# Kernel tuning notes

Measured on AMD Instinct MI355X. Metric: run time of the kernel, lower is better.

The kernel has to match this reference:

```python
import jax, jax.numpy as jnp
import numpy as np

NS = 100000  # senders
NR = 100000  # receivers
E = 600000   # edges
D = 128      # sender_dim = receiver_dim = edge_dim
EPS = 1e-5


def _layer_norm(x, g, b):
    mu = jnp.mean(x, axis=-1, keepdims=True)
    var = jnp.mean(jnp.square(x - mu), axis=-1, keepdims=True)
    return (x - mu) * jax.lax.rsqrt(var + EPS) * g + b


def _gcast_mlp(x, W, b, gamma, beta):
    # Faithful to GCastMLP.forward: z = silu(linear(x)); z = LN(silu(z))
    z = jax.nn.silu(x @ W.T + b)
    return _layer_norm(jax.nn.silu(z), gamma, beta)


def setup_inputs() -> dict:
    key = jax.random.key(0)
    ks = jax.random.split(key, 12)
    s = 1.0 / np.sqrt(3 * D)
    inp = {
        "sender_x": jax.random.normal(ks[0], (NS, D), jnp.float32),
        "receiver_x": jax.random.normal(ks[1], (NR, D), jnp.float32),
        "edge_index": jax.random.randint(ks[2], (2, E), 0, NR, jnp.int32),
        "edge_attr": jax.random.normal(ks[3], (E, D), jnp.float32),
        # edge MLP: in = sender+receiver+edge = 3D, out = edge_dim
        "We": jax.random.uniform(ks[4], (D, 3 * D), jnp.float32, -s, s),
        "be": jnp.zeros((D,), jnp.float32),
        "ge": jnp.ones((D,), jnp.float32),
        "bbe": jnp.zeros((D,), jnp.float32),
        # node MLP: in = receiver+edge = 2D, out = receiver_dim
        "Wn": jax.random.uniform(ks[5], (D, 2 * D), jnp.float32, -1.0 / np.sqrt(2 * D), 1.0 / np.sqrt(2 * D)),
        "bn": jnp.zeros((D,), jnp.float32),
        "gn": jnp.ones((D,), jnp.float32),
        "bbn": jnp.zeros((D,), jnp.float32),
        # sender MLP: square D -> D
        "Ws": jax.random.uniform(ks[6], (D, D), jnp.float32, -1.0 / np.sqrt(D), 1.0 / np.sqrt(D)),
        "bs": jnp.zeros((D,), jnp.float32),
        "gs": jnp.ones((D,), jnp.float32),
        "bbs": jnp.zeros((D,), jnp.float32),
    }
    return inp


def reference(sender_x, receiver_x, edge_index, edge_attr,
              We, be, ge, bbe, Wn, bn, gn, bbn, Ws, bs, gs, bbs):
    src, dst = edge_index[0], edge_index[1]
    # Edge encoder: gather endpoints, concat, MLP -> new edge features [E, D]
    edge_in = jnp.concatenate([sender_x[src], receiver_x[dst], edge_attr], axis=-1)
    edge_attr_p = _gcast_mlp(edge_in, We, be, ge, bbe)
    # Node encoder: scatter-sum messages (= new edge features) to receivers
    edge_aggr = jax.ops.segment_sum(edge_attr_p, dst, num_segments=receiver_x.shape[0])
    mesh_x_p = _gcast_mlp(jnp.concatenate([receiver_x, edge_aggr], axis=-1), Wn, bn, gn, bbn)
    # Residual updates
    sender_out = sender_x + _gcast_mlp(sender_x, Ws, bs, gs, bbs)
    receiver_out = receiver_x + mesh_x_p
    edge_out = edge_attr + edge_attr_p
    return (sender_out, receiver_out, edge_out)
```

## Files before the change

kernel.cpp:

```cpp
#include <hip/hip_runtime.h>
#include <stdint.h>


typedef __bf16 bf16x8 __attribute__((ext_vector_type(8)));
typedef float  f32x4  __attribute__((ext_vector_type(4)));

union U16B { uint4 u; bf16x8 v; };
union BFPK { __bf16 h[2]; unsigned int u; };
union BF1  { __bf16 h; unsigned short s; };

__device__ __forceinline__ float silu_f(float x) {
  return x * __builtin_amdgcn_rcpf(1.0f + __expf(-x));
}
__device__ __forceinline__ float bfu2f(unsigned int lo16) {
  return __uint_as_float(lo16 << 16);
}
__device__ __forceinline__ bf16x8 cvt8(float4 a, float4 b) {
  bf16x8 r;
  r[0] = (__bf16)a.x; r[1] = (__bf16)a.y; r[2] = (__bf16)a.z; r[3] = (__bf16)a.w;
  r[4] = (__bf16)b.x; r[5] = (__bf16)b.y; r[6] = (__bf16)b.z; r[7] = (__bf16)b.w;
  return r;
}

__global__ void prep_kernel(const float* __restrict__ We,
                            const float* __restrict__ Wn,
                            const float* __restrict__ Ws,
                            unsigned short* __restrict__ wimg,
                            const float* __restrict__ sx,
                            unsigned short* __restrict__ sb,
                            const float* __restrict__ rx,
                            unsigned short* __restrict__ rb,
                            int n8s, int n8r,
                            const int* __restrict__ dst,
                            int* __restrict__ counts, int E) {
  int i = blockIdx.x * 256 + threadIdx.x;
  if (i < 6 * 16384) {
    int panel = i >> 14;
    int r = (i >> 7) & 127;
    int csw = i & 127;
    int c_or = ((csw * 2) ^ ((r & 15) << 4)) >> 1;
    float f;
    if (panel < 3)      f = We[r * 384 + panel * 128 + c_or];
    else if (panel < 5) f = Wn[r * 256 + (panel - 3) * 128 + c_or];
    else                f = Ws[r * 128 + c_or];
    BF1 c; c.h = (__bf16)f;
    wimg[i] = c.s;
    return;
  }
  int j = i - 6 * 16384;
  if (j < n8s + n8r) {
    const float* in; unsigned short* out; int idx;
    if (j < n8s) { in = sx; out = sb; idx = j; }
    else         { in = rx; out = rb; idx = j - n8s; }
    float4 a = reinterpret_cast<const float4*>(in)[2 * idx];
    float4 b = reinterpret_cast<const float4*>(in)[2 * idx + 1];
    U16B r8; r8.v = cvt8(a, b);
    reinterpret_cast<uint4*>(out)[idx] = r8.u;
    return;
  }
  int e = j - n8s - n8r;
  if (e < E) atomicAdd(&counts[dst[e]], 1);
}

__global__ void scan1_kernel(const int* __restrict__ counts, int* __restrict__ pre,
                             int* __restrict__ blockSums, int n) {
  __shared__ int sh[256];
  const int t = threadIdx.x;
  const int base = blockIdx.x * 1024 + t * 4;
  int c0 = (base + 0 < n) ? counts[base + 0] : 0;
  int c1 = (base + 1 < n) ? counts[base + 1] : 0;
  int c2 = (base + 2 < n) ? counts[base + 2] : 0;
  int c3 = (base + 3 < n) ? counts[base + 3] : 0;
  int tot = c0 + c1 + c2 + c3;
  sh[t] = tot;
  __syncthreads();
  #pragma unroll
  for (int off = 1; off < 256; off <<= 1) {
    int v = (t >= off) ? sh[t - off] : 0;
    __syncthreads();
    sh[t] += v;
    __syncthreads();
  }
  int excl = sh[t] - tot;
  if (base + 0 < n) pre[base + 0] = excl;
  if (base + 1 < n) pre[base + 1] = excl + c0;
  if (base + 2 < n) pre[base + 2] = excl + c0 + c1;
  if (base + 3 < n) pre[base + 3] = excl + c0 + c1 + c2;
  if (t == 255) blockSums[blockIdx.x] = sh[255];
}

__global__ void scan2_kernel(int* __restrict__ blockSums, int nb) {
  __shared__ int sh[512];
  const int t = threadIdx.x;
  int v = (t < nb) ? blockSums[t] : 0;
  sh[t] = v;
  __syncthreads();
  #pragma unroll
  for (int off = 1; off < 512; off <<= 1) {
    int u = (t >= off) ? sh[t - off] : 0;
    __syncthreads();
    sh[t] += u;
    __syncthreads();
  }
  if (t < nb) blockSums[t] = sh[t] - v;
}

__global__ void scan3_kernel(const int* __restrict__ pre, const int* __restrict__ blockSums,
                             int* __restrict__ offs, int* __restrict__ cursor, int n) {
  int i = blockIdx.x * 256 + threadIdx.x;
  if (i >= n) return;
  int o = pre[i] + blockSums[i >> 10];
  offs[i] = o;
  cursor[i] = o;
}

__global__ void scatter_kernel(const int* __restrict__ dst, int* __restrict__ cursor,
                               int* __restrict__ rank, int E) {
  int i = blockIdx.x * 256 + threadIdx.x;
  if (i < E) {
    int p = atomicAdd(&cursor[dst[i]], 1);
    rank[i] = p;
  }
}

template <int KDIM, int AGGR>
__device__ __forceinline__ void mlp_core(
    unsigned short* smem,
    const unsigned short* __restrict__ s0, const int* __restrict__ i0,
    const unsigned short* __restrict__ s1, const int* __restrict__ i1,
    const float* __restrict__ s2,
    const unsigned short* __restrict__ Wb,
    const float* __restrict__ bias, const float* __restrict__ gamma,
    const float* __restrict__ beta,
    const float* __restrict__ resid,
    float* __restrict__ outp,
    void* aggr, const int* __restrict__ aggr_idx,
    const int* __restrict__ prank,
    int M, int bid) {
  constexpr int NSEG = KDIM / 128;

  const int tid = threadIdx.x;
  const int wid = tid >> 6;
  const int lane = tid & 63;
  const int l15 = lane & 15;
  const int q = lane >> 4;
  const int l31 = lane & 31;
  const int rhalf = lane >> 5;
  const int wrow = bid * 128 + wid * 16;
  const int xm = l15 << 3;

  int rr = wrow + l15;
  if (rr >= M) rr = M - 1;
  const unsigned short* p0 = s0 + (size_t)(i0 ? i0[rr] : rr) * 128;
  const unsigned short* p1 = nullptr;
  const float* p2 = nullptr;
  if constexpr (KDIM >= 256) p1 = s1 + (size_t)(i1 ? i1[rr] : rr) * 128;
  if constexpr (KDIM >= 384) p2 = s2 + (size_t)rr * 128;

  auto stageB = [&](int seg) {
    const unsigned short* g = Wb + seg * 16384 + wid * 2048 + lane * 8;
    unsigned short* l = &smem[wid * 2048];
    #pragma unroll
    for (int u = 0; u < 4; ++u) {
      __builtin_amdgcn_global_load_lds(
          (const __attribute__((address_space(1))) unsigned int*)(g + u * 512),
          (__attribute__((address_space(3))) unsigned int*)(l + u * 512),
          16, 0, 0);
    }
  };

  U16B Ac[4], An[4];
  auto loadA = [&](int seg, U16B (&dst)[4]) {
    #pragma unroll
    for (int k4 = 0; k4 < 4; ++k4) {
      const int kof = k4 * 32 + q * 8;
      if (seg == 0) {
        dst[k4].u = *reinterpret_cast<const uint4*>(p0 + kof);
      } else if (seg == 1) {
        dst[k4].u = *reinterpret_cast<const uint4*>(p1 + kof);
      } else {
        const float4* p = reinterpret_cast<const float4*>(p2 + kof);
        dst[k4].v = cvt8(p[0], p[1]);
      }
    }
  };

  f32x4 acc[8] = {};

  stageB(0);
  loadA(0, Ac);
  __syncthreads();

  #pragma unroll
  for (int seg = 0; seg < NSEG; ++seg) {
    if (seg + 1 < NSEG) loadA(seg + 1, An);
    #pragma unroll
    for (int k4 = 0; k4 < 4; ++k4) {
      #pragma unroll
      for (int n = 0; n < 8; ++n) {
        U16B b;
        b.u = *reinterpret_cast<const uint4*>(
            &smem[(n * 16 + l15) * 128 + ((k4 * 32 + q * 8) ^ xm)]);
        acc[n] = __builtin_amdgcn_mfma_f32_16x16x32_bf16(Ac[k4].v, b.v, acc[n], 0, 0, 0);
      }
    }
    __syncthreads();
    if (seg + 1 < NSEG) {
      stageB(seg + 1);
      __syncthreads();
      #pragma unroll
      for (int k4 = 0; k4 < 4; ++k4) Ac[k4] = An[k4];
    }
  }

  float bia[8];
  #pragma unroll
  for (int n = 0; n < 8; ++n) bia[n] = bias[n * 16 + l15];

  float sum[4] = {0.f, 0.f, 0.f, 0.f};
  float ssq[4] = {0.f, 0.f, 0.f, 0.f};
  #pragma unroll
  for (int n = 0; n < 8; ++n) {
    #pragma unroll
    for (int j = 0; j < 4; ++j) {
      float t = silu_f(silu_f(acc[n][j] + bia[n]));
      acc[n][j] = t;
      sum[j] += t;
      ssq[j] += t * t;
    }
  }
  #pragma unroll
  for (int off = 1; off < 16; off <<= 1) {
    #pragma unroll
    for (int j = 0; j < 4; ++j) {
      sum[j] += __shfl_xor(sum[j], off);
      ssq[j] += __shfl_xor(ssq[j], off);
    }
  }
  float mu[4], rs[4];
  #pragma unroll
  for (int j = 0; j < 4; ++j) {
    mu[j] = sum[j] * (1.0f / 128.0f);
    float var = ssq[j] * (1.0f / 128.0f) - mu[j] * mu[j];
    rs[j] = rsqrtf(var + 1e-5f);
  }
  float gam[8], bet[8];
  #pragma unroll
  for (int n = 0; n < 8; ++n) {
    gam[n] = gamma[n * 16 + l15];
    bet[n] = beta[n * 16 + l15];
  }

  unsigned short* yw = &smem[wid * 2048];

  #pragma unroll
  for (int h = 0; h < 2; ++h) {
    if (h == 1) {
      asm volatile("s_waitcnt lgkmcnt(0)" ::: "memory");
    }
    if ((q >> 1) == h) {
      #pragma unroll
      for (int n = 0; n < 8; ++n) {
        #pragma unroll
        for (int j = 0; j < 4; ++j) {
          float y = (acc[n][j] - mu[j]) * rs[j] * gam[n] + bet[n];
          BF1 c; c.h = (__bf16)y;
          yw[((q & 1) * 4 + j) * 132 + n * 16 + l15] = c.s;
        }
      }
    }
    asm volatile("s_waitcnt lgkmcnt(0)" ::: "memory");

    #pragma unroll
    for (int s = 0; s < 4; ++s) {
      int row8 = 2 * s + rhalf;
      int grow = wrow + 8 * h + row8;
      uint2 w = *reinterpret_cast<const uint2*>(&yw[row8 * 132 + l31 * 4]);
      if (grow < M) {
        const f32x4 r4 = *reinterpret_cast<const f32x4*>(resid + (size_t)grow * 128 + l31 * 4);
        f32x4 o4;
        o4.x = r4.x + bfu2f(w.x & 0xffffu);
        o4.y = r4.y + bfu2f(w.x >> 16);
        o4.z = r4.z + bfu2f(w.y & 0xffffu);
        o4.w = r4.w + bfu2f(w.y >> 16);
        __builtin_nontemporal_store(o4, reinterpret_cast<f32x4*>(outp + (size_t)grow * 128 + l31 * 4));
        if constexpr (AGGR == 3) {
          int prow = prank[grow];
          *reinterpret_cast<uint2*>((unsigned short*)aggr + (size_t)prow * 128 + l31 * 4) = w;
        } else if constexpr (AGGR == 2) {
          int idx = aggr_idx[grow];
          unsigned short* ar = (unsigned short*)aggr + (size_t)idx * 128 + l31 * 4;
          asm volatile("global_atomic_pk_add_bf16 %0, %1, off" :: "v"(ar), "v"(w.x) : "memory");
          asm volatile("global_atomic_pk_add_bf16 %0, %1, off" :: "v"(ar + 2), "v"(w.y) : "memory");
        }
      }
    }
  }
}

template <int KDIM, int AGGR>
__global__ __launch_bounds__(512, 6) void mlp_v10_kernel(
    const unsigned short* __restrict__ s0, const int* __restrict__ i0,
    const unsigned short* __restrict__ s1, const int* __restrict__ i1,
    const float* __restrict__ s2,
    const unsigned short* __restrict__ Wb,
    const float* __restrict__ bias, const float* __restrict__ gamma,
    const float* __restrict__ beta,
    const float* __restrict__ resid,
    float* __restrict__ outp,
    void* aggr, const int* __restrict__ aggr_idx,
    const int* __restrict__ prank,
    int M) {
  __shared__ __align__(16) unsigned short smem[16384];
  mlp_core<KDIM, AGGR>(smem, s0, i0, s1, i1, s2, Wb, bias, gamma, beta,
                       resid, outp, aggr, aggr_idx, prank, M, blockIdx.x);
}

__global__ __launch_bounds__(512, 6) void fused_es_kernel(
    const unsigned short* __restrict__ sender_b, const int* __restrict__ src,
    const unsigned short* __restrict__ receiver_b, const int* __restrict__ dst,
    const float* __restrict__ edge_attr,
    const unsigned short* __restrict__ We_b,
    const float* __restrict__ be, const float* __restrict__ ge,
    const float* __restrict__ bbe,
    float* __restrict__ edge_out,
    unsigned short* __restrict__ P, const int* __restrict__ rank,
    const unsigned short* __restrict__ Ws_b,
    const float* __restrict__ bs, const float* __restrict__ gs,
    const float* __restrict__ bbs,
    const float* __restrict__ sender_x, float* __restrict__ sender_out,
    int E, int NS, int gridE) {
  __shared__ __align__(16) unsigned short smem[16384];
  const int b = blockIdx.x;
  if (b < gridE) {
    mlp_core<384, 3>(smem, sender_b, src, receiver_b, dst, edge_attr,
                     We_b, be, ge, bbe, edge_attr, edge_out,
                     P, nullptr, rank, E, b);
  } else {
    mlp_core<128, 0>(smem, sender_b, nullptr, nullptr, nullptr, nullptr,
                     Ws_b, bs, gs, bbs, sender_x, sender_out,
                     nullptr, nullptr, nullptr, NS, b - gridE);
  }
}

__global__ __launch_bounds__(512, 4) void node_csr_kernel(
    const unsigned short* __restrict__ s0,
    const unsigned short* __restrict__ P,
    const int* __restrict__ offs, const int* __restrict__ counts,
    const unsigned short* __restrict__ Wb,
    const float* __restrict__ bias, const float* __restrict__ gamma,
    const float* __restrict__ beta,
    const float* __restrict__ resid, float* __restrict__ outp,
    int M) {
  __shared__ __align__(16) unsigned short smem[16384];

  const int tid = threadIdx.x;
  const int wid = tid >> 6;
  const int lane = tid & 63;
  const int l15 = lane & 15;
  const int q = lane >> 4;
  const int l31 = lane & 31;
  const int rhalf = lane >> 5;
  const int wrow = blockIdx.x * 128 + wid * 16;
  const int xm = l15 << 3;

  int rr = wrow + l15;
  if (rr >= M) rr = M - 1;
  const unsigned short* p0 = s0 + (size_t)rr * 128;

  auto stageB = [&](int seg) {
    const unsigned short* g = Wb + seg * 16384 + wid * 2048 + lane * 8;
    unsigned short* l = &smem[wid * 2048];
    #pragma unroll
    for (int u = 0; u < 4; ++u) {
      __builtin_amdgcn_global_load_lds(
          (const __attribute__((address_space(1))) unsigned int*)(g + u * 512),
          (__attribute__((address_space(3))) unsigned int*)(l + u * 512),
          16, 0, 0);
    }
  };

  U16B Ac[4];
  #pragma unroll
  for (int k4 = 0; k4 < 4; ++k4)
    Ac[k4].u = *reinterpret_cast<const uint4*>(p0 + k4 * 32 + q * 8);

  stageB(0);
  __syncthreads();

  f32x4 acc[8] = {};
  #pragma unroll
  for (int k4 = 0; k4 < 4; ++k4) {
    #pragma unroll
    for (int n = 0; n < 8; ++n) {
      U16B b;
      b.u = *reinterpret_cast<const uint4*>(
          &smem[(n * 16 + l15) * 128 + ((k4 * 32 + q * 8) ^ xm)]);
      acc[n] = __builtin_amdgcn_mfma_f32_16x16x32_bf16(Ac[k4].v, b.v, acc[n], 0, 0, 0);
    }
  }
  __syncthreads();
  stageB(1);

  {
    int beg = offs[rr];
    int cnt = counts[rr];
    float a32[32];
    #pragma unroll
    for (int t = 0; t < 32; ++t) a32[t] = 0.f;
    const unsigned short* prow = P + (size_t)beg * 128;
    for (int k = 0; k < cnt; ++k) {
      #pragma unroll
      for (int k4 = 0; k4 < 4; ++k4) {
        uint4 w = *reinterpret_cast<const uint4*>(prow + k4 * 32 + q * 8);
        a32[k4 * 8 + 0] += bfu2f(w.x & 0xffffu);
        a32[k4 * 8 + 1] += bfu2f(w.x >> 16);
        a32[k4 * 8 + 2] += bfu2f(w.y & 0xffffu);
        a32[k4 * 8 + 3] += bfu2f(w.y >> 16);
        a32[k4 * 8 + 4] += bfu2f(w.z & 0xffffu);
        a32[k4 * 8 + 5] += bfu2f(w.z >> 16);
        a32[k4 * 8 + 6] += bfu2f(w.w & 0xffffu);
        a32[k4 * 8 + 7] += bfu2f(w.w >> 16);
      }
      prow += 128;
    }
    #pragma unroll
    for (int k4 = 0; k4 < 4; ++k4) {
      #pragma unroll
      for (int j = 0; j < 8; ++j)
        Ac[k4].v[j] = (__bf16)a32[k4 * 8 + j];
    }
  }
  __syncthreads();

  #pragma unroll
  for (int k4 = 0; k4 < 4; ++k4) {
    #pragma unroll
    for (int n = 0; n < 8; ++n) {
      U16B b;
      b.u = *reinterpret_cast<const uint4*>(
          &smem[(n * 16 + l15) * 128 + ((k4 * 32 + q * 8) ^ xm)]);
      acc[n] = __builtin_amdgcn_mfma_f32_16x16x32_bf16(Ac[k4].v, b.v, acc[n], 0, 0, 0);
    }
  }
  __syncthreads();

  float bia[8];
  #pragma unroll
  for (int n = 0; n < 8; ++n) bia[n] = bias[n * 16 + l15];

  float sum[4] = {0.f, 0.f, 0.f, 0.f};
  float ssq[4] = {0.f, 0.f, 0.f, 0.f};
  #pragma unroll
  for (int n = 0; n < 8; ++n) {
    #pragma unroll
    for (int j = 0; j < 4; ++j) {
      float t = silu_f(silu_f(acc[n][j] + bia[n]));
      acc[n][j] = t;
      sum[j] += t;
      ssq[j] += t * t;
    }
  }
  #pragma unroll
  for (int off = 1; off < 16; off <<= 1) {
    #pragma unroll
    for (int j = 0; j < 4; ++j) {
      sum[j] += __shfl_xor(sum[j], off);
      ssq[j] += __shfl_xor(ssq[j], off);
    }
  }
  float mu[4], rs[4];
  #pragma unroll
  for (int j = 0; j < 4; ++j) {
    mu[j] = sum[j] * (1.0f / 128.0f);
    float var = ssq[j] * (1.0f / 128.0f) - mu[j] * mu[j];
    rs[j] = rsqrtf(var + 1e-5f);
  }
  float gam[8], bet[8];
  #pragma unroll
  for (int n = 0; n < 8; ++n) {
    gam[n] = gamma[n * 16 + l15];
    bet[n] = beta[n * 16 + l15];
  }

  unsigned short* yw = &smem[wid * 2048];

  #pragma unroll
  for (int h = 0; h < 2; ++h) {
    if (h == 1) {
      asm volatile("s_waitcnt lgkmcnt(0)" ::: "memory");
    }
    if ((q >> 1) == h) {
      #pragma unroll
      for (int n = 0; n < 8; ++n) {
        #pragma unroll
        for (int j = 0; j < 4; ++j) {
          float y = (acc[n][j] - mu[j]) * rs[j] * gam[n] + bet[n];
          BF1 c; c.h = (__bf16)y;
          yw[((q & 1) * 4 + j) * 132 + n * 16 + l15] = c.s;
        }
      }
    }
    asm volatile("s_waitcnt lgkmcnt(0)" ::: "memory");

    #pragma unroll
    for (int s = 0; s < 4; ++s) {
      int row8 = 2 * s + rhalf;
      int grow = wrow + 8 * h + row8;
      uint2 w = *reinterpret_cast<const uint2*>(&yw[row8 * 132 + l31 * 4]);
      if (grow < M) {
        const f32x4 r4 = *reinterpret_cast<const f32x4*>(resid + (size_t)grow * 128 + l31 * 4);
        f32x4 o4;
        o4.x = r4.x + bfu2f(w.x & 0xffffu);
        o4.y = r4.y + bfu2f(w.x >> 16);
        o4.z = r4.z + bfu2f(w.y & 0xffffu);
        o4.w = r4.w + bfu2f(w.y >> 16);
        __builtin_nontemporal_store(o4, reinterpret_cast<f32x4*>(outp + (size_t)grow * 128 + l31 * 4));
      }
    }
  }
}

template <int KDIM>
__global__ __launch_bounds__(512, 4) void mlp_fb_kernel(
    const float* __restrict__ s0, const int* __restrict__ i0,
    const float* __restrict__ s1, const int* __restrict__ i1,
    const float* __restrict__ s2,
    const unsigned short* __restrict__ Wb,
    const float* __restrict__ bias, const float* __restrict__ gamma,
    const float* __restrict__ beta,
    const float* __restrict__ resid,
    float* __restrict__ outp,
    float* aggr, const int* __restrict__ aggr_idx,
    int M) {
  constexpr int NSEG = KDIM / 128;
  __shared__ __align__(16) unsigned short smem[2][16384];
  const int tid = threadIdx.x;
  const int wid = tid >> 6;
  const int lane = tid & 63;
  const int l15 = lane & 15;
  const int q = lane >> 4;
  const int l31 = lane & 31;
  const int rhalf = lane >> 5;
  const int wrow = blockIdx.x * 128 + wid * 16;
  const int xm = l15 << 3;

  int rr = wrow + l15;
  if (rr >= M) rr = M - 1;
  const float* p0 = s0 + (size_t)(i0 ? i0[rr] : rr) * 128;
  const float* p1 = (KDIM >= 256) ? (s1 + (size_t)(i1 ? i1[rr] : rr) * 128) : nullptr;
  const float* p2 = (KDIM >= 384) ? (s2 + (size_t)rr * 128) : nullptr;

  auto stageB = [&](int seg, int buf) {
    const unsigned short* g = Wb + seg * 16384 + wid * 2048 + lane * 8;
    unsigned short* l = &smem[buf][wid * 2048];
    #pragma unroll
    for (int u = 0; u < 4; ++u) {
      __builtin_amdgcn_global_load_lds(
          (const __attribute__((address_space(1))) unsigned int*)(g + u * 512),
          (__attribute__((address_space(3))) unsigned int*)(l + u * 512),
          16, 0, 0);
    }
  };

  stageB(0, 0);
  f32x4 acc[8] = {};
  __syncthreads();
  int cur = 0;
  #pragma unroll
  for (int seg = 0; seg < NSEG; ++seg) {
    if (seg + 1 < NSEG) stageB(seg + 1, cur ^ 1);
    const float* base = (seg == 0) ? p0 : ((seg == 1) ? p1 : p2);
    #pragma unroll
    for (int k4 = 0; k4 < 4; ++k4) {
      const float4* pp = reinterpret_cast<const float4*>(base + k4 * 32 + q * 8);
      U16B a; a.v = cvt8(pp[0], pp[1]);
      #pragma unroll
      for (int n = 0; n < 8; ++n) {
        U16B b;
        b.u = *reinterpret_cast<const uint4*>(
            &smem[cur][(n * 16 + l15) * 128 + ((k4 * 32 + q * 8) ^ xm)]);
        acc[n] = __builtin_amdgcn_mfma_f32_16x16x32_bf16(a.v, b.v, acc[n], 0, 0, 0);
      }
    }
    __syncthreads();
    if (seg + 1 < NSEG) cur ^= 1;
  }

  unsigned short* yw = &smem[0][0] + wid * (16 * 132);
  float bia[8];
  #pragma unroll
  for (int n = 0; n < 8; ++n) bia[n] = bias[n * 16 + l15];
  float sum[4] = {0.f, 0.f, 0.f, 0.f}, ssq[4] = {0.f, 0.f, 0.f, 0.f};
  #pragma unroll
  for (int n = 0; n < 8; ++n)
    #pragma unroll
    for (int j = 0; j < 4; ++j) {
      float t = silu_f(silu_f(acc[n][j] + bia[n]));
      acc[n][j] = t; sum[j] += t; ssq[j] += t * t;
    }
  #pragma unroll
  for (int off = 1; off < 16; off <<= 1)
    #pragma unroll
    for (int j = 0; j < 4; ++j) {
      sum[j] += __shfl_xor(sum[j], off);
      ssq[j] += __shfl_xor(ssq[j], off);
    }
  float mu[4], rs[4];
  #pragma unroll
  for (int j = 0; j < 4; ++j) {
    mu[j] = sum[j] * (1.0f / 128.0f);
    float var = ssq[j] * (1.0f / 128.0f) - mu[j] * mu[j];
    rs[j] = rsqrtf(var + 1e-5f);
  }
  float gam[8], bet[8];
  #pragma unroll
  for (int n = 0; n < 8; ++n) { gam[n] = gamma[n * 16 + l15]; bet[n] = beta[n * 16 + l15]; }
  #pragma unroll
  for (int n = 0; n < 8; ++n)
    #pragma unroll
    for (int j = 0; j < 4; ++j) {
      float y = (acc[n][j] - mu[j]) * rs[j] * gam[n] + bet[n];
      BF1 c; c.h = (__bf16)y;
      yw[(q * 4 + j) * 132 + n * 16 + l15] = c.s;
    }
  asm volatile("s_waitcnt lgkmcnt(0)" ::: "memory");
  #pragma unroll
  for (int s = 0; s < 8; ++s) {
    int row16 = 2 * s + rhalf;
    int grow = wrow + row16;
    uint2 w = *reinterpret_cast<const uint2*>(&yw[row16 * 132 + l31 * 4]);
    if (grow < M) {
      const f32x4 r4 = *reinterpret_cast<const f32x4*>(resid + (size_t)grow * 128 + l31 * 4);
      f32x4 o4;
      o4.x = r4.x + bfu2f(w.x & 0xffffu);
      o4.y = r4.y + bfu2f(w.x >> 16);
      o4.z = r4.z + bfu2f(w.y & 0xffffu);
      o4.w = r4.w + bfu2f(w.y >> 16);
      __builtin_nontemporal_store(o4, reinterpret_cast<f32x4*>(outp + (size_t)grow * 128 + l31 * 4));
      if (aggr) {
        int idx = aggr_idx[grow];
        float* ar = aggr + (size_t)idx * 128 + l31 * 4;
        atomicAdd(ar + 0, bfu2f(w.x & 0xffffu));
        atomicAdd(ar + 1, bfu2f(w.x >> 16));
        atomicAdd(ar + 2, bfu2f(w.y & 0xffffu));
        atomicAdd(ar + 3, bfu2f(w.y >> 16));
      }
    }
  }
}

extern "C" void kernel_launch(void* const* d_in, const int* in_sizes, int n_in,
                              void* d_out, int out_size, void* d_ws, size_t ws_size,
                              hipStream_t stream) {
  const float* sender_x   = (const float*)d_in[0];
  const float* receiver_x = (const float*)d_in[1];
  const int*   edge_index = (const int*)d_in[2];
  const float* edge_attr  = (const float*)d_in[3];
  const float* We  = (const float*)d_in[4];
  const float* be  = (const float*)d_in[5];
  const float* ge  = (const float*)d_in[6];
  const float* bbe = (const float*)d_in[7];
  const float* Wn  = (const float*)d_in[8];
  const float* bn  = (const float*)d_in[9];
  const float* gn  = (const float*)d_in[10];
  const float* bbn = (const float*)d_in[11];
  const float* Ws  = (const float*)d_in[12];
  const float* bs  = (const float*)d_in[13];
  const float* gs  = (const float*)d_in[14];
  const float* bbs = (const float*)d_in[15];

  const int D  = 128;
  const int NS = in_sizes[0] / D;
  const int NR = in_sizes[1] / D;
  const int E  = in_sizes[2] / 2;

  const int* src = edge_index;
  const int* dst = edge_index + E;

  float* out          = (float*)d_out;
  float* sender_out   = out;
  float* receiver_out = out + (size_t)NS * D;
  float* edge_out     = out + (size_t)(NS + NR) * D;

  const size_t welems = 6 * 16384;
  unsigned short* We_b = (unsigned short*)d_ws;
  unsigned short* Wn_b = We_b + 3 * 16384;
  unsigned short* Ws_b = We_b + 5 * 16384;
  unsigned short* sender_b   = We_b + welems;
  unsigned short* receiver_b = sender_b + (size_t)NS * D;
  unsigned short* aggr_b     = receiver_b + (size_t)NR * D;
  unsigned short* P_b        = aggr_b + (size_t)NR * D;
  int* counts    = (int*)(P_b + (size_t)E * D);
  int* pre       = counts + NR;
  int* offs      = pre + NR;
  int* cursor    = offs + NR;
  int* blockSums = cursor + NR;
  int* rank      = blockSums + 512;

  const int nScanBlocks = (NR + 1023) / 1024;
  const size_t needCSR = 2 * (welems + (size_t)(NS + 2 * NR) * D + (size_t)E * D)
                       + 4 * (4 * (size_t)NR + 512 + (size_t)E);
  const size_t needA = (welems + (size_t)(NS + 2 * NR) * D) * 2;

  int tier;
  if (ws_size >= needCSR && nScanBlocks <= 512) tier = 0;
  else if (ws_size >= needA) tier = 1;
  else tier = 2;

  const int gridE = (E + 127) / 128;
  const int gridR = (NR + 127) / 128;
  const int gridS = (NS + 127) / 128;
  const int n8s = NS * D / 8, n8r = NR * D / 8;

  if (tier == 0) {
    (void)hipMemsetAsync(counts, 0, (size_t)NR * 4, stream);
    const int prepItems = (int)welems + n8s + n8r + E;
    prep_kernel<<<(prepItems + 255) / 256, 256, 0, stream>>>(
        We, Wn, Ws, We_b, sender_x, sender_b, receiver_x, receiver_b,
        n8s, n8r, dst, counts, E);

    scan1_kernel<<<nScanBlocks, 256, 0, stream>>>(counts, pre, blockSums, NR);
    scan2_kernel<<<1, 512, 0, stream>>>(blockSums, nScanBlocks);
    scan3_kernel<<<(NR + 255) / 256, 256, 0, stream>>>(pre, blockSums, offs, cursor, NR);
    scatter_kernel<<<(E + 255) / 256, 256, 0, stream>>>(dst, cursor, rank, E);

    fused_es_kernel<<<gridE + gridS, 512, 0, stream>>>(
        sender_b, src, receiver_b, dst, edge_attr,
        We_b, be, ge, bbe, edge_out, P_b, rank,
        Ws_b, bs, gs, bbs, sender_x, sender_out,
        E, NS, gridE);

    node_csr_kernel<<<gridR, 512, 0, stream>>>(
        receiver_b, P_b, offs, counts,
        Wn_b, bn, gn, bbn, receiver_x, receiver_out, NR);
  } else if (tier == 1) {
    const int prepItems = (int)welems + n8s + n8r;
    prep_kernel<<<(prepItems + 255) / 256, 256, 0, stream>>>(
        We, Wn, Ws, We_b, sender_x, sender_b, receiver_x, receiver_b,
        n8s, n8r, nullptr, nullptr, 0);
    (void)hipMemsetAsync(aggr_b, 0, (size_t)NR * D * 2, stream);

    mlp_v10_kernel<384, 2><<<gridE, 512, 0, stream>>>(
        sender_b, src, receiver_b, dst, edge_attr,
        We_b, be, ge, bbe, edge_attr, edge_out, aggr_b, dst, nullptr, E);

    mlp_v10_kernel<256, 0><<<gridR, 512, 0, stream>>>(
        receiver_b, nullptr, aggr_b, nullptr, nullptr,
        Wn_b, bn, gn, bbn, receiver_x, receiver_out, nullptr, nullptr, nullptr, NR);

    mlp_v10_kernel<128, 0><<<gridS, 512, 0, stream>>>(
        sender_b, nullptr, nullptr, nullptr, nullptr,
        Ws_b, bs, gs, bbs, sender_x, sender_out, nullptr, nullptr, nullptr, NS);
  } else {
    prep_kernel<<<(int)((welems + 255) / 256), 256, 0, stream>>>(
        We, Wn, Ws, We_b, nullptr, nullptr, nullptr, nullptr, 0, 0,
        nullptr, nullptr, 0);
    (void)hipMemsetAsync(receiver_out, 0, (size_t)NR * D * sizeof(float), stream);

    mlp_fb_kernel<384><<<gridE, 512, 0, stream>>>(
        sender_x, src, receiver_x, dst, edge_attr,
        We_b, be, ge, bbe, edge_attr, edge_out, receiver_out, dst, E);

    mlp_fb_kernel<256><<<gridR, 512, 0, stream>>>(
        receiver_x, nullptr, receiver_out, nullptr, nullptr,
        Wn_b, bn, gn, bbn, receiver_x, receiver_out, nullptr, nullptr, NR);

    mlp_fb_kernel<128><<<gridS, 512, 0, stream>>>(
        sender_x, nullptr, nullptr, nullptr, nullptr,
        Ws_b, bs, gs, bbs, sender_x, sender_out, nullptr, nullptr, NS);
  }
}
```

Before: 451.4 us.

## Process edges in destination-sorted order via inverse permutation

The scatter kernel now writes an inverse permutation (sorted slot -> edge id) instead of each edge's rank. The edge MLP then walks rows in dst-sorted order, gathering inputs and residuals through the permutation and writing P contiguously. The goal is locality: consecutive rows share receiver rows and the P writes are coalesced. In exchange, edge_attr reads and edge_out writes become scattered, and there is one extra indirection per row.

```diff
diff --git a/kernel.cpp b/kernel.cpp
--- a/kernel.cpp
+++ b/kernel.cpp
@@ -115,15 +115,15 @@
 }
 
 __global__ void scatter_kernel(const int* __restrict__ dst, int* __restrict__ cursor,
-                               int* __restrict__ rank, int E) {
+                               int* __restrict__ eorder, int E) {
   int i = blockIdx.x * 256 + threadIdx.x;
   if (i < E) {
     int p = atomicAdd(&cursor[dst[i]], 1);
-    rank[i] = p;
-  }
-}
-
-template <int KDIM, int AGGR>
+    eorder[p] = i;
+  }
+}
+
+template <int KDIM, int AGGR, bool SORTED>
 __device__ __forceinline__ void mlp_core(
     unsigned short* smem,
     const unsigned short* __restrict__ s0, const int* __restrict__ i0,
@@ -135,7 +135,7 @@
     const float* __restrict__ resid,
     float* __restrict__ outp,
     void* aggr, const int* __restrict__ aggr_idx,
-    const int* __restrict__ prank,
+    const int* __restrict__ perm,
     int M, int bid) {
   constexpr int NSEG = KDIM / 128;
 
@@ -151,11 +151,13 @@
 
   int rr = wrow + l15;
   if (rr >= M) rr = M - 1;
-  const unsigned short* p0 = s0 + (size_t)(i0 ? i0[rr] : rr) * 128;
+  int ridx = rr;
+  if constexpr (SORTED) ridx = perm[rr];
+  const unsigned short* p0 = s0 + (size_t)(i0 ? i0[ridx] : ridx) * 128;
   const unsigned short* p1 = nullptr;
   const float* p2 = nullptr;
-  if constexpr (KDIM >= 256) p1 = s1 + (size_t)(i1 ? i1[rr] : rr) * 128;
-  if constexpr (KDIM >= 384) p2 = s2 + (size_t)rr * 128;
+  if constexpr (KDIM >= 256) p1 = s1 + (size_t)(i1 ? i1[ridx] : ridx) * 128;
+  if constexpr (KDIM >= 384) p2 = s2 + (size_t)ridx * 128;
 
   auto stageB = [&](int seg) {
     const unsigned short* g = Wb + seg * 16384 + wid * 2048 + lane * 8;
@@ -170,17 +172,17 @@
   };
 
   U16B Ac[4], An[4];
-  auto loadA = [&](int seg, U16B (&dst)[4]) {
+  auto loadA = [&](int seg, U16B (&dst_)[4]) {
     #pragma unroll
     for (int k4 = 0; k4 < 4; ++k4) {
       const int kof = k4 * 32 + q * 8;
       if (seg == 0) {
-        dst[k4].u = *reinterpret_cast<const uint4*>(p0 + kof);
+        dst_[k4].u = *reinterpret_cast<const uint4*>(p0 + kof);
       } else if (seg == 1) {
-        dst[k4].u = *reinterpret_cast<const uint4*>(p1 + kof);
+        dst_[k4].u = *reinterpret_cast<const uint4*>(p1 + kof);
       } else {
         const float4* p = reinterpret_cast<const float4*>(p2 + kof);
-        dst[k4].v = cvt8(p[0], p[1]);
+        dst_[k4].v = cvt8(p[0], p[1]);
       }
     }
   };
@@ -277,15 +279,17 @@
       int grow = wrow + 8 * h + row8;
       uint2 w = *reinterpret_cast<const uint2*>(&yw[row8 * 132 + l31 * 4]);
       if (grow < M) {
-        const f32x4 r4 = *reinterpret_cast<const f32x4*>(resid + (size_t)grow * 128 + l31 * 4);
+        int og = grow;
+        if constexpr (SORTED) og = perm[grow];
+        const f32x4 r4 = *reinterpret_cast<const f32x4*>(resid + (size_t)og * 128 + l31 * 4);
         f32x4 o4;
         o4.x = r4.x + bfu2f(w.x & 0xffffu);
         o4.y = r4.y + bfu2f(w.x >> 16);
         o4.z = r4.z + bfu2f(w.y & 0xffffu);
         o4.w = r4.w + bfu2f(w.y >> 16);
-        __builtin_nontemporal_store(o4, reinterpret_cast<f32x4*>(outp + (size_t)grow * 128 + l31 * 4));
+        __builtin_nontemporal_store(o4, reinterpret_cast<f32x4*>(outp + (size_t)og * 128 + l31 * 4));
         if constexpr (AGGR == 3) {
-          int prow = prank[grow];
+          int prow = SORTED ? grow : perm[grow];
           *reinterpret_cast<uint2*>((unsigned short*)aggr + (size_t)prow * 128 + l31 * 4) = w;
         } else if constexpr (AGGR == 2) {
           int idx = aggr_idx[grow];
@@ -312,8 +316,8 @@
     const int* __restrict__ prank,
     int M) {
   __shared__ __align__(16) unsigned short smem[16384];
-  mlp_core<KDIM, AGGR>(smem, s0, i0, s1, i1, s2, Wb, bias, gamma, beta,
-                       resid, outp, aggr, aggr_idx, prank, M, blockIdx.x);
+  mlp_core<KDIM, AGGR, false>(smem, s0, i0, s1, i1, s2, Wb, bias, gamma, beta,
+                              resid, outp, aggr, aggr_idx, prank, M, blockIdx.x);
 }
 
 __global__ __launch_bounds__(512, 6) void fused_es_kernel(
@@ -324,7 +328,7 @@
     const float* __restrict__ be, const float* __restrict__ ge,
     const float* __restrict__ bbe,
     float* __restrict__ edge_out,
-    unsigned short* __restrict__ P, const int* __restrict__ rank,
+    unsigned short* __restrict__ P, const int* __restrict__ eorder,
     const unsigned short* __restrict__ Ws_b,
     const float* __restrict__ bs, const float* __restrict__ gs,
     const float* __restrict__ bbs,
@@ -333,13 +337,13 @@
   __shared__ __align__(16) unsigned short smem[16384];
   const int b = blockIdx.x;
   if (b < gridE) {
-    mlp_core<384, 3>(smem, sender_b, src, receiver_b, dst, edge_attr,
-                     We_b, be, ge, bbe, edge_attr, edge_out,
-                     P, nullptr, rank, E, b);
+    mlp_core<384, 3, true>(smem, sender_b, src, receiver_b, dst, edge_attr,
+                           We_b, be, ge, bbe, edge_attr, edge_out,
+                           P, nullptr, eorder, E, b);
   } else {
-    mlp_core<128, 0>(smem, sender_b, nullptr, nullptr, nullptr, nullptr,
-                     Ws_b, bs, gs, bbs, sender_x, sender_out,
-                     nullptr, nullptr, nullptr, NS, b - gridE);
+    mlp_core<128, 0, false>(smem, sender_b, nullptr, nullptr, nullptr, nullptr,
+                            Ws_b, bs, gs, bbs, sender_x, sender_out,
+                            nullptr, nullptr, nullptr, NS, b - gridE);
   }
 }
 
@@ -696,7 +700,7 @@
   int* offs      = pre + NR;
   int* cursor    = offs + NR;
   int* blockSums = cursor + NR;
-  int* rank      = blockSums + 512;
+  int* eorder    = blockSums + 512;
 
   const int nScanBlocks = (NR + 1023) / 1024;
   const size_t needCSR = 2 * (welems + (size_t)(NS + 2 * NR) * D + (size_t)E * D)
@@ -723,11 +727,11 @@
     scan1_kernel<<<nScanBlocks, 256, 0, stream>>>(counts, pre, blockSums, NR);
     scan2_kernel<<<1, 512, 0, stream>>>(blockSums, nScanBlocks);
     scan3_kernel<<<(NR + 255) / 256, 256, 0, stream>>>(pre, blockSums, offs, cursor, NR);
-    scatter_kernel<<<(E + 255) / 256, 256, 0, stream>>>(dst, cursor, rank, E);
+    scatter_kernel<<<(E + 255) / 256, 256, 0, stream>>>(dst, cursor, eorder, E);
 
     fused_es_kernel<<<gridE + gridS, 512, 0, stream>>>(
         sender_b, src, receiver_b, dst, edge_attr,
-        We_b, be, ge, bbe, edge_out, P_b, rank,
+        We_b, be, ge, bbe, edge_out, P_b, eorder,
         Ws_b, bs, gs, bbs, sender_x, sender_out,
         E, NS, gridE);
 
```

Measured after the change: 468.1 us. +3.7%, slower.
